# Performance work log

Hardware: AMD Instinct MI355X
Metric: run time of the kernel (lower is better)

## Reference

```python
import jax, jax.numpy as jnp
import numpy as np

N_NODES = 100000
N_EDGES = 1600000
C_IN = 128
C_OUT = 128
BN_EPS = 1e-5


def setup_inputs() -> dict:
    key = jax.random.key(0)
    k = jax.random.split(key, 4)
    x = jax.random.normal(k[0], (N_NODES, C_IN), dtype=jnp.float32)
    edge_index = jax.random.randint(k[1], (2, N_EDGES), 0, N_NODES, dtype=jnp.int32)
    # nn.Linear params (Kaiming-uniform-ish scale)
    lim = 1.0 / np.sqrt(C_IN)
    W = jax.random.uniform(k[2], (C_IN, C_OUT), jnp.float32, -lim, lim)
    b = jnp.zeros((C_OUT,), jnp.float32)
    # BatchNorm (eval mode: running stats)
    gamma = jnp.ones((C_OUT,), jnp.float32)
    beta = jnp.zeros((C_OUT,), jnp.float32)
    running_mean = jnp.zeros((C_OUT,), jnp.float32)
    running_var = jnp.ones((C_OUT,), jnp.float32)
    return {"x": x, "edge_index": edge_index, "W": W, "b": b,
            "gamma": gamma, "beta": beta,
            "running_mean": running_mean, "running_var": running_var}


def reference(x, edge_index, W, b, gamma, beta, running_mean, running_var):
    # Linear projection: [N, C_in] @ [C_in, C_out]
    h = x @ W + b
    in_node, out_node = edge_index[0], edge_index[1]
    # gather edge features then scatter-mean onto destination nodes
    sums = jax.ops.segment_sum(h[in_node], out_node, num_segments=N_NODES)
    cnt = jax.ops.segment_sum(jnp.ones((in_node.shape[0],), h.dtype), out_node,
                              num_segments=N_NODES)
    agg = sums / jnp.maximum(cnt, 1.0)[:, None]  # mean; 0 for isolated nodes
    # BatchNorm1d (eval mode: running stats) + ReLU; dropout is identity in eval
    inv = jax.lax.rsqrt(running_var + BN_EPS)
    out = (agg - running_mean) * (inv * gamma) + beta
    return jax.nn.relu(out)
```

## Files before the change

kernel.cpp:

```cpp
#include <hip/hip_runtime.h>


#define NN 100000
#define NE 1600000
#define CC 128
#define BN_EPS 1e-5f
#define LBLK 1563
#define LSTR 136
#define NBUK 256
#define DPB 391
#define ACH 4096
#define ABLK 391
#define CAP 10240

typedef __attribute__((ext_vector_type(8))) short bf16x8;
typedef __attribute__((ext_vector_type(4))) float f32x4;

static __device__ __forceinline__ short f2bf(float f) {
  union { float f; unsigned u; } v; v.f = f;
  unsigned r = (v.u + 0x7FFF + ((v.u >> 16) & 1)) >> 16;
  return (short)r;
}
static __device__ __forceinline__ float bflo(unsigned p) {
  return __uint_as_float(p << 16);
}
static __device__ __forceinline__ float bfhi(unsigned p) {
  return __uint_as_float(p & 0xffff0000u);
}

static __device__ __forceinline__ int excl_scan256(int* a, int t, int v) {
  a[t] = v;
  __syncthreads();
  for (int d = 1; d < 256; d <<= 1) {
    const int x = (t >= d) ? a[t - d] : 0;
    __syncthreads();
    a[t] += x;
    __syncthreads();
  }
  const int incl = a[t];
  __syncthreads();
  a[t] = incl - v;
  __syncthreads();
  return incl - v;
}

__global__ __launch_bounds__(256) void prep_hist(
    const float* __restrict__ W, const float* __restrict__ bias,
    const float* __restrict__ gamma, const float* __restrict__ beta,
    const float* __restrict__ rmean, const float* __restrict__ rvar,
    const int* __restrict__ ei, short* __restrict__ Wsw,
    float* __restrict__ scsh, int* __restrict__ bhist) {
  __shared__ int lh[NBUK];
  const int t = threadIdx.x;
  const int i = blockIdx.x * 256 + t;
  if (i < CC * CC) {
    const int k = i >> 7, n = i & 127;
    const int nt = n & 7, m = n >> 3;
    const int kb = k >> 5, q = (k >> 3) & 3, j = k & 7;
    Wsw[(size_t)(((nt * 4 + kb) * 64 + (m + 16 * q)) * 8 + j)] = f2bf(W[i]);
  }
  if (i < CC) {
    const float sc = gamma[i] * rsqrtf(rvar[i] + BN_EPS);
    scsh[i] = sc;
    scsh[CC + i] = beta[i] - rmean[i] * sc;
    scsh[2 * CC + i] = bias[i];
  }
  lh[t] = 0;
  __syncthreads();
  const int e0 = blockIdx.x * ACH;
  const int e1 = min(NE, e0 + ACH);
  for (int e = e0 + t; e < e1; e += 256) atomicAdd(&lh[ei[NE + e] / DPB], 1);
  __syncthreads();
  if (lh[t]) atomicAdd(&bhist[t], lh[t]);
}

__global__ __launch_bounds__(256) void scatter_linear(
    const int* __restrict__ ei, const int* __restrict__ bhist,
    int* __restrict__ gcurz, int2* __restrict__ ebuf,
    const float* __restrict__ x, const short* __restrict__ Wsw,
    const float* __restrict__ scsh, short* __restrict__ hout,
    int scat) {
  __shared__ int2 sorted[ACH];
  __shared__ int gsc[NBUK], lh[NBUK], lex[NBUK], rb[NBUK], lc[NBUK];
  const int t = threadIdx.x;

  if (blockIdx.x < scat) {
    const int e0 = blockIdx.x * ACH;
    const int e1 = min(NE, e0 + ACH);
    const int gbase = excl_scan256(gsc, t, bhist[t]);
    lh[t] = 0;
    __syncthreads();
    for (int e = e0 + t; e < e1; e += 256) atomicAdd(&lh[ei[NE + e] / DPB], 1);
    __syncthreads();
    const int vh = lh[t];
    const int lbase = excl_scan256(lex, t, vh);
    lc[t] = lbase;
    if (vh > 0) rb[t] = gbase + atomicAdd(&gcurz[t], vh);
    __syncthreads();
    for (int e = e0 + t; e < e1; e += 256) {
      const int src = ei[e], dst = ei[NE + e];
      const int p = atomicAdd(&lc[dst / DPB], 1);
      sorted[p] = make_int2(src, dst);
    }
    __syncthreads();
    const int n = e1 - e0;
    for (int i = t; i < n; i += 256) {
      const int2 v = sorted[i];
      const int b = v.y / DPB;
      ebuf[rb[b] + (i - lex[b])] = v;
    }
    return;
  }

  short* lsA = (short*)sorted;
  const int n0 = (blockIdx.x - scat) * 64;

#pragma unroll
  for (int j = 0; j < 8; ++j) {
    const int idx = j * 256 + t;
    const int row = idx >> 5, kc4 = idx & 31;
    float4 v = make_float4(0.f, 0.f, 0.f, 0.f);
    if (n0 + row < NN) v = *(const float4*)(x + (size_t)(n0 + row) * CC + kc4 * 4);
    short4 sv;
    sv.x = f2bf(v.x); sv.y = f2bf(v.y); sv.z = f2bf(v.z); sv.w = f2bf(v.w);
    *(short4*)(lsA + row * LSTR + kc4 * 4) = sv;
  }
  __syncthreads();

  const int wave = t >> 6, lane = t & 63;
  const int quad = lane >> 4, m = lane & 15;
  const int rowbase = n0 + wave * 16;

  f32x4 acc[8];
#pragma unroll
  for (int nt = 0; nt < 8; ++nt) acc[nt] = (f32x4){0.f, 0.f, 0.f, 0.f};

#pragma unroll
  for (int kb = 0; kb < 4; ++kb) {
    const bf16x8 a =
        *(const bf16x8*)(lsA + (wave * 16 + m) * LSTR + kb * 32 + quad * 8);
#pragma unroll
    for (int nt = 0; nt < 8; ++nt) {
      bf16x8 bb = *(const bf16x8*)(Wsw + (size_t)(((nt * 4 + kb) * 64 + lane) * 8));
      acc[nt] = __builtin_amdgcn_mfma_f32_16x16x32_bf16(a, bb, acc[nt], 0, 0, 0);
    }
  }

  const float4 b0 = *(const float4*)(scsh + 2 * CC + m * 8);
  const float4 b1 = *(const float4*)(scsh + 2 * CC + m * 8 + 4);
  const float bv[8] = {b0.x, b0.y, b0.z, b0.w, b1.x, b1.y, b1.z, b1.w};

  short* hg = hout + (size_t)(m >> 1) * (NN * 16) + (m & 1) * 8;
#pragma unroll
  for (int reg = 0; reg < 4; ++reg) {
    const int R = rowbase + quad * 4 + reg;
    if (R >= NN) continue;
    bf16x8 hv;
#pragma unroll
    for (int nt = 0; nt < 8; ++nt) hv[nt] = f2bf(acc[nt][reg] + bv[nt]);
    *(bf16x8*)(hg + (size_t)R * 16) = hv;
  }
}

__global__ __launch_bounds__(1024) void bucket_to_csr(
    const int2* __restrict__ ebuf, const int* __restrict__ bhist,
    int* __restrict__ off, int* __restrict__ csr) {
  __shared__ int gs[NBUK];
  __shared__ int dh[512];
  __shared__ int s[512];
  __shared__ int lcur[512];
  __shared__ int lcsr[CAP];
  const int b = blockIdx.x, t = threadIdx.x;

  if (t < NBUK) gs[t] = bhist[t];
  __syncthreads();
  for (int d = 1; d < NBUK; d <<= 1) {
    int a0 = 0;
    if (t < NBUK && t >= d) a0 = gs[t - d];
    __syncthreads();
    if (t < NBUK) gs[t] += a0;
    __syncthreads();
  }
  const int seglen = bhist[b];
  const int segbase = gs[b] - seglen;
  const int lo = b * DPB;
  const int hi = min(NN, lo + DPB);
  const int nd = hi - lo;
  const int2* eb = ebuf + segbase;

  if (t < 512) dh[t] = 0;
  __syncthreads();
  for (int i = t; i < seglen; i += 1024) atomicAdd(&dh[eb[i].y - lo], 1);
  __syncthreads();

  if (t < 512) s[t] = dh[t];
  __syncthreads();
  for (int d = 1; d < 512; d <<= 1) {
    int a0 = 0;
    if (t < 512 && t >= d) a0 = s[t - d];
    __syncthreads();
    if (t < 512) s[t] += a0;
    __syncthreads();
  }
  if (t < 512) lcur[t] = s[t] - dh[t];
  if (t < nd) off[lo + t] = segbase + (s[t] - dh[t]);
  if (b == NBUK - 1 && t == 0) off[NN] = NE;
  __syncthreads();

  if (seglen <= CAP) {
    for (int i = t; i < seglen; i += 1024) {
      const int2 e = eb[i];
      const int p = atomicAdd(&lcur[e.y - lo], 1);
      lcsr[p] = e.x;
    }
    __syncthreads();
    for (int i = t; i < seglen; i += 1024) csr[segbase + i] = lcsr[i];
  } else {
    for (int i = t; i < seglen; i += 1024) {
      const int2 e = eb[i];
      const int p = atomicAdd(&lcur[e.y - lo], 1);
      csr[segbase + p] = e.x;
    }
  }
}

__global__ __launch_bounds__(256) void gather_bn_relu(
    const short* __restrict__ h, const int* __restrict__ off,
    const int* __restrict__ csr, const float* __restrict__ scsh,
    float* __restrict__ out) {
  const int g = blockIdx.x & 7;
  const int wave = threadIdx.x >> 6, lane = threadIdx.x & 63;
  const int o = lane >> 3, c8 = lane & 7;
  const int node = (blockIdx.x >> 3) * 32 + wave * 8 + o;
  const unsigned* hb = (const unsigned*)h + (size_t)g * (NN * 8) + c8;

  int s = 0, e = 0;
  if (node < NN) { s = off[node]; e = off[node + 1]; }

  float ax = 0.f, ay = 0.f;
  int i = s;
  for (; i + 4 <= e; i += 4) {
    const int s0 = csr[i + 0], s1 = csr[i + 1];
    const int s2 = csr[i + 2], s3 = csr[i + 3];
    const unsigned p0 = hb[(size_t)s0 * 8];
    const unsigned p1 = hb[(size_t)s1 * 8];
    const unsigned p2 = hb[(size_t)s2 * 8];
    const unsigned p3 = hb[(size_t)s3 * 8];
    ax += (bflo(p0) + bflo(p1)) + (bflo(p2) + bflo(p3));
    ay += (bfhi(p0) + bfhi(p1)) + (bfhi(p2) + bfhi(p3));
  }
  for (; i < e; ++i) {
    const unsigned p = hb[(size_t)csr[i] * 8];
    ax += bflo(p);
    ay += bfhi(p);
  }
  if (node < NN) {
    const float inv = (e > s) ? 1.0f / (float)(e - s) : 0.0f;
    const int cidx = g * 16 + c8 * 2;
    const float2 sc = *(const float2*)(scsh + cidx);
    const float2 sh = *(const float2*)(scsh + CC + cidx);
    float2 o2;
    o2.x = fmaxf(0.f, ax * inv * sc.x + sh.x);
    o2.y = fmaxf(0.f, ay * inv * sc.y + sh.y);
    *(float2*)(out + (size_t)node * CC + cidx) = o2;
  }
}

__global__ __launch_bounds__(256) void edge_scatter(
    const float* __restrict__ x, const int* __restrict__ ei,
    float* __restrict__ sums, int* __restrict__ cnt) {
  int gt = blockIdx.x * 256 + threadIdx.x;
  int e = gt >> 5;
  int sub = gt & 31;
  if (e >= NE) return;
  int src = ei[e];
  int dst = ei[NE + e];
  const float4 v = *(const float4*)(x + (size_t)src * CC + sub * 4);
  float* o = sums + (size_t)dst * CC + sub * 4;
  unsafeAtomicAdd(o + 0, v.x);
  unsafeAtomicAdd(o + 1, v.y);
  unsafeAtomicAdd(o + 2, v.z);
  unsafeAtomicAdd(o + 3, v.w);
  if (sub == 0) atomicAdd(cnt + dst, 1);
}

__global__ __launch_bounds__(256) void gemm_bn_relu_fb(
    float* buf, const float* __restrict__ W, const float* __restrict__ bias,
    const float* __restrict__ gamma, const float* __restrict__ beta,
    const float* __restrict__ rmean, const float* __restrict__ rvar,
    const int* __restrict__ cnt) {
  __shared__ float xsT[CC][65];
  const int t = threadIdx.x;
  const int n0 = blockIdx.x * 64;
  for (int j = 0; j < 8; ++j) {
    int i = t + 256 * j;
    int row = i >> 5;
    int ko = (i & 31) * 4;
    float4 v = make_float4(0.f, 0.f, 0.f, 0.f);
    if (n0 + row < NN) v = *(const float4*)(buf + (size_t)(n0 + row) * CC + ko);
    xsT[ko + 0][row] = v.x;
    xsT[ko + 1][row] = v.y;
    xsT[ko + 2][row] = v.z;
    xsT[ko + 3][row] = v.w;
  }
  __syncthreads();
  const int cg = t & 31;
  const int ng8 = (t >> 5) * 8;
  float acc[8][4];
#pragma unroll
  for (int j = 0; j < 8; ++j)
#pragma unroll
    for (int c = 0; c < 4; ++c) acc[j][c] = 0.f;
#pragma unroll 8
  for (int k = 0; k < CC; ++k) {
    const float4 wv = *(const float4*)(W + k * CC + cg * 4);
#pragma unroll
    for (int j = 0; j < 8; ++j) {
      const float xv = xsT[k][ng8 + j];
      acc[j][0] = fmaf(xv, wv.x, acc[j][0]);
      acc[j][1] = fmaf(xv, wv.y, acc[j][1]);
      acc[j][2] = fmaf(xv, wv.z, acc[j][2]);
      acc[j][3] = fmaf(xv, wv.w, acc[j][3]);
    }
  }
  const float4 bb = *(const float4*)(bias + cg * 4);
  const float4 gg = *(const float4*)(gamma + cg * 4);
  const float4 bt = *(const float4*)(beta + cg * 4);
  const float4 mu = *(const float4*)(rmean + cg * 4);
  const float4 vr = *(const float4*)(rvar + cg * 4);
  float sc[4], sh[4];
  sc[0] = gg.x * rsqrtf(vr.x + BN_EPS);
  sc[1] = gg.y * rsqrtf(vr.y + BN_EPS);
  sc[2] = gg.z * rsqrtf(vr.z + BN_EPS);
  sc[3] = gg.w * rsqrtf(vr.w + BN_EPS);
  sh[0] = bt.x - mu.x * sc[0];
  sh[1] = bt.y - mu.y * sc[1];
  sh[2] = bt.z - mu.z * sc[2];
  sh[3] = bt.w - mu.w * sc[3];
#pragma unroll
  for (int j = 0; j < 8; ++j) {
    const int n = n0 + ng8 + j;
    if (n >= NN) continue;
    const int cn = cnt[n];
    const float inv = cn > 0 ? 1.0f / (float)cn : 0.0f;
    const float bsel = cn > 0 ? 1.0f : 0.0f;
    float4 o;
    o.x = fmaxf(0.f, (acc[j][0] * inv + bsel * bb.x) * sc[0] + sh[0]);
    o.y = fmaxf(0.f, (acc[j][1] * inv + bsel * bb.y) * sc[1] + sh[1]);
    o.z = fmaxf(0.f, (acc[j][2] * inv + bsel * bb.z) * sc[2] + sh[2]);
    o.w = fmaxf(0.f, (acc[j][3] * inv + bsel * bb.w) * sc[3] + sh[3]);
    *(float4*)(buf + (size_t)n * CC + cg * 4) = o;
  }
}

extern "C" void kernel_launch(void* const* d_in, const int* in_sizes, int n_in,
                              void* d_out, int out_size, void* d_ws, size_t ws_size,
                              hipStream_t stream) {
  const float* x     = (const float*)d_in[0];
  const int*   ei    = (const int*)d_in[1];
  const float* W     = (const float*)d_in[2];
  const float* bias  = (const float*)d_in[3];
  const float* gamma = (const float*)d_in[4];
  const float* beta  = (const float*)d_in[5];
  const float* rmean = (const float*)d_in[6];
  const float* rvar  = (const float*)d_in[7];
  float* out = (float*)d_out;

  const size_t OFF_B  = 0;
  const size_t BH_B   = 400128;
  const size_t GC_B   = 401152;
  const size_t CSR_B  = 802304;
  const size_t SCSH_B = 7202304;
  const size_t WSW_B  = 7204352;
  const size_t EB_B   = 7237120;
  const size_t H1_B   = 20037120;
  const size_t NEED1  = H1_B + (size_t)NN * CC * 2;
  const size_t NEED2  = EB_B + (size_t)NN * CC * 2;

  const int GGRID = ((NN + 31) / 32) * 8;

  if (ws_size >= NEED2) {
    int*   off   = (int*)((char*)d_ws + OFF_B);
    int*   bhist = (int*)((char*)d_ws + BH_B);
    int*   gcurz = (int*)((char*)d_ws + GC_B);
    int*   csr   = (int*)((char*)d_ws + CSR_B);
    float* scsh  = (float*)((char*)d_ws + SCSH_B);
    short* Wsw   = (short*)((char*)d_ws + WSW_B);

    hipMemsetAsync(bhist, 0, 2048, stream);
    prep_hist<<<ABLK, 256, 0, stream>>>(W, bias, gamma, beta, rmean, rvar,
                                        ei, Wsw, scsh, bhist);
    if (ws_size >= NEED1) {
      int2*  ebuf = (int2*)((char*)d_ws + EB_B);
      short* h    = (short*)((char*)d_ws + H1_B);
      scatter_linear<<<ABLK + LBLK, 256, 0, stream>>>(
          ei, bhist, gcurz, ebuf, x, Wsw, scsh, h, ABLK);
      bucket_to_csr<<<NBUK, 1024, 0, stream>>>(ebuf, bhist, off, csr);
      gather_bn_relu<<<GGRID, 256, 0, stream>>>(h, off, csr, scsh, out);
    } else {
      int2*  ebuf = (int2*)((char*)d_ws + EB_B);
      short* h    = (short*)((char*)d_ws + EB_B);
      scatter_linear<<<ABLK, 256, 0, stream>>>(
          ei, bhist, gcurz, ebuf, x, Wsw, scsh, h, ABLK);
      bucket_to_csr<<<NBUK, 1024, 0, stream>>>(ebuf, bhist, off, csr);
      scatter_linear<<<LBLK, 256, 0, stream>>>(
          ei, bhist, gcurz, ebuf, x, Wsw, scsh, h, 0);
      gather_bn_relu<<<GGRID, 256, 0, stream>>>(h, off, csr, scsh, out);
    }
  } else {
    int* cnt = (int*)d_ws;
    hipMemsetAsync(out, 0, (size_t)NN * CC * sizeof(float), stream);
    hipMemsetAsync(cnt, 0, (size_t)NN * sizeof(int), stream);
    edge_scatter<<<(NE * 32) / 256, 256, 0, stream>>>(x, ei, out, cnt);
    gemm_bn_relu_fb<<<(NN + 63) / 64, 256, 0, stream>>>(
        out, W, bias, gamma, beta, rmean, rvar, cnt);
  }
}
```

Measured before the change: 255.3 us.

## Stage CSR segments in LDS and widen per-thread gather in aggregation kernel

Measured after the change: 238.7 us. -6.5%, faster.

```diff
diff --git a/kernel.cpp b/kernel.cpp
--- a/kernel.cpp
+++ b/kernel.cpp
@@ -12,6 +12,8 @@
 #define ACH 4096
 #define ABLK 391
 #define CAP 10240
+#define GNB 256
+#define CAP2 5120
 
 typedef __attribute__((ext_vector_type(8))) short bf16x8;
 typedef __attribute__((ext_vector_type(4))) float f32x4;
@@ -129,7 +131,6 @@
 
   const int wave = t >> 6, lane = t & 63;
   const int quad = lane >> 4, m = lane & 15;
-  const int rowbase = n0 + wave * 16;
 
   f32x4 acc[8];
 #pragma unroll
@@ -150,15 +151,28 @@
   const float4 b1 = *(const float4*)(scsh + 2 * CC + m * 8 + 4);
   const float bv[8] = {b0.x, b0.y, b0.z, b0.w, b1.x, b1.y, b1.z, b1.w};
 
-  short* hg = hout + (size_t)(m >> 1) * (NN * 16) + (m & 1) * 8;
+  __syncthreads();
+
 #pragma unroll
   for (int reg = 0; reg < 4; ++reg) {
-    const int R = rowbase + quad * 4 + reg;
-    if (R >= NN) continue;
+    const int r = wave * 16 + quad * 4 + reg;
     bf16x8 hv;
 #pragma unroll
     for (int nt = 0; nt < 8; ++nt) hv[nt] = f2bf(acc[nt][reg] + bv[nt]);
-    *(bf16x8*)(hg + (size_t)R * 16) = hv;
+    *(bf16x8*)(lsA + r * LSTR + m * 8) = hv;
+  }
+  __syncthreads();
+
+#pragma unroll
+  for (int rr = 0; rr < 4; ++rr) {
+    const int g2 = rr * 2 + (t >> 7);
+    const int idx = t & 127;
+    const int row = idx >> 1, half = idx & 1;
+    const int R = n0 + row;
+    if (R < NN) {
+      bf16x8 v = *(const bf16x8*)(lsA + row * LSTR + g2 * 16 + half * 8);
+      *(bf16x8*)(hout + (size_t)g2 * (NN * 16) + (size_t)R * 16 + half * 8) = v;
+    }
   }
 }
 
@@ -228,41 +242,83 @@
     const short* __restrict__ h, const int* __restrict__ off,
     const int* __restrict__ csr, const float* __restrict__ scsh,
     float* __restrict__ out) {
+  __shared__ int loff[GNB + 1];
+  __shared__ int lcsr[CAP2];
   const int g = blockIdx.x & 7;
-  const int wave = threadIdx.x >> 6, lane = threadIdx.x & 63;
-  const int o = lane >> 3, c8 = lane & 7;
-  const int node = (blockIdx.x >> 3) * 32 + wave * 8 + o;
-  const unsigned* hb = (const unsigned*)h + (size_t)g * (NN * 8) + c8;
-
-  int s = 0, e = 0;
-  if (node < NN) { s = off[node]; e = off[node + 1]; }
-
-  float ax = 0.f, ay = 0.f;
-  int i = s;
-  for (; i + 4 <= e; i += 4) {
-    const int s0 = csr[i + 0], s1 = csr[i + 1];
-    const int s2 = csr[i + 2], s3 = csr[i + 3];
-    const unsigned p0 = hb[(size_t)s0 * 8];
-    const unsigned p1 = hb[(size_t)s1 * 8];
-    const unsigned p2 = hb[(size_t)s2 * 8];
-    const unsigned p3 = hb[(size_t)s3 * 8];
-    ax += (bflo(p0) + bflo(p1)) + (bflo(p2) + bflo(p3));
-    ay += (bfhi(p0) + bfhi(p1)) + (bfhi(p2) + bfhi(p3));
-  }
-  for (; i < e; ++i) {
-    const unsigned p = hb[(size_t)csr[i] * 8];
-    ax += bflo(p);
-    ay += bfhi(p);
-  }
-  if (node < NN) {
-    const float inv = (e > s) ? 1.0f / (float)(e - s) : 0.0f;
-    const int cidx = g * 16 + c8 * 2;
-    const float2 sc = *(const float2*)(scsh + cidx);
-    const float2 sh = *(const float2*)(scsh + CC + cidx);
-    float2 o2;
-    o2.x = fmaxf(0.f, ax * inv * sc.x + sh.x);
-    o2.y = fmaxf(0.f, ay * inv * sc.y + sh.y);
-    *(float2*)(out + (size_t)node * CC + cidx) = o2;
+  const int nb0 = (blockIdx.x >> 3) * GNB;
+  const int t = threadIdx.x;
+  const int nnb = min(GNB, NN - nb0);
+
+  for (int i = t; i <= nnb; i += 256) loff[i] = off[nb0 + i];
+  __syncthreads();
+  const int s0 = loff[0];
+  const int seglen = loff[nnb] - s0;
+  const int stg = min(seglen, CAP2);
+  for (int i = t; i < stg; i += 256) lcsr[i] = csr[s0 + i];
+  __syncthreads();
+
+  const int c4 = t & 3;
+  const int lgid = t >> 2;
+  const short* hg = h + (size_t)g * (NN * 16);
+  const float4 sc = *(const float4*)(scsh + g * 16 + c4 * 4);
+  const float4 sh = *(const float4*)(scsh + CC + g * 16 + c4 * 4);
+
+  if (seglen <= CAP2) {
+#pragma unroll
+    for (int nn = 0; nn < 4; ++nn) {
+      const int l = lgid * 4 + nn;
+      if (l < nnb) {
+        const int s = loff[l] - s0, e = loff[l + 1] - s0;
+        float a0 = 0.f, a1 = 0.f, a2 = 0.f, a3 = 0.f;
+        int i = s;
+        for (; i + 4 <= e; i += 4) {
+          const int e0 = lcsr[i], e1 = lcsr[i + 1];
+          const int e2 = lcsr[i + 2], e3 = lcsr[i + 3];
+          const uint2 p0 = *(const uint2*)(hg + (size_t)e0 * 16 + c4 * 4);
+          const uint2 p1 = *(const uint2*)(hg + (size_t)e1 * 16 + c4 * 4);
+          const uint2 p2 = *(const uint2*)(hg + (size_t)e2 * 16 + c4 * 4);
+          const uint2 p3 = *(const uint2*)(hg + (size_t)e3 * 16 + c4 * 4);
+          a0 += (bflo(p0.x) + bflo(p1.x)) + (bflo(p2.x) + bflo(p3.x));
+          a1 += (bfhi(p0.x) + bfhi(p1.x)) + (bfhi(p2.x) + bfhi(p3.x));
+          a2 += (bflo(p0.y) + bflo(p1.y)) + (bflo(p2.y) + bflo(p3.y));
+          a3 += (bfhi(p0.y) + bfhi(p1.y)) + (bfhi(p2.y) + bfhi(p3.y));
+        }
+        for (; i < e; ++i) {
+          const uint2 p = *(const uint2*)(hg + (size_t)lcsr[i] * 16 + c4 * 4);
+          a0 += bflo(p.x); a1 += bfhi(p.x);
+          a2 += bflo(p.y); a3 += bfhi(p.y);
+        }
+        const int node = nb0 + l;
+        const float inv = (e > s) ? 1.0f / (float)(e - s) : 0.0f;
+        float4 o;
+        o.x = fmaxf(0.f, a0 * inv * sc.x + sh.x);
+        o.y = fmaxf(0.f, a1 * inv * sc.y + sh.y);
+        o.z = fmaxf(0.f, a2 * inv * sc.z + sh.z);
+        o.w = fmaxf(0.f, a3 * inv * sc.w + sh.w);
+        *(float4*)(out + (size_t)node * CC + g * 16 + c4 * 4) = o;
+      }
+    }
+  } else {
+    for (int nn = 0; nn < 4; ++nn) {
+      const int l = lgid * 4 + nn;
+      if (l < nnb) {
+        const int s = loff[l], e = loff[l + 1];
+        float a0 = 0.f, a1 = 0.f, a2 = 0.f, a3 = 0.f;
+        for (int i = s; i < e; ++i) {
+          const uint2 p = *(const uint2*)(hg + (size_t)csr[i] * 16 + c4 * 4);
+          a0 += bflo(p.x); a1 += bfhi(p.x);
+          a2 += bflo(p.y); a3 += bfhi(p.y);
+        }
+        const int node = nb0 + l;
+        const float inv = (e > s) ? 1.0f / (float)(e - s) : 0.0f;
+        float4 o;
+        o.x = fmaxf(0.f, a0 * inv * sc.x + sh.x);
+        o.y = fmaxf(0.f, a1 * inv * sc.y + sh.y);
+        o.z = fmaxf(0.f, a2 * inv * sc.z + sh.z);
+        o.w = fmaxf(0.f, a3 * inv * sc.w + sh.w);
+        *(float4*)(out + (size_t)node * CC + g * 16 + c4 * 4) = o;
+      }
+    }
   }
 }
 
@@ -377,7 +433,7 @@
   const size_t NEED1  = H1_B + (size_t)NN * CC * 2;
   const size_t NEED2  = EB_B + (size_t)NN * CC * 2;
 
-  const int GGRID = ((NN + 31) / 32) * 8;
+  const int GGRID = ((NN + GNB - 1) / GNB) * 8;
 
   if (ws_size >= NEED2) {
     int*   off   = (int*)((char*)d_ws + OFF_B);
```

## Store h row-major and gather full 256-byte rows per edge with staged CSR

Applied to the files above, without the earlier changes.

Measured after the change: 222.3 us. 1.15x faster.

```diff
diff --git a/kernel.cpp b/kernel.cpp
--- a/kernel.cpp
+++ b/kernel.cpp
@@ -12,6 +12,8 @@
 #define ACH 4096
 #define ABLK 391
 #define CAP 10240
+#define GNB 64
+#define CAP2 1536
 
 typedef __attribute__((ext_vector_type(8))) short bf16x8;
 typedef __attribute__((ext_vector_type(4))) float f32x4;
@@ -150,7 +152,6 @@
   const float4 b1 = *(const float4*)(scsh + 2 * CC + m * 8 + 4);
   const float bv[8] = {b0.x, b0.y, b0.z, b0.w, b1.x, b1.y, b1.z, b1.w};
 
-  short* hg = hout + (size_t)(m >> 1) * (NN * 16) + (m & 1) * 8;
 #pragma unroll
   for (int reg = 0; reg < 4; ++reg) {
     const int R = rowbase + quad * 4 + reg;
@@ -158,7 +159,7 @@
     bf16x8 hv;
 #pragma unroll
     for (int nt = 0; nt < 8; ++nt) hv[nt] = f2bf(acc[nt][reg] + bv[nt]);
-    *(bf16x8*)(hg + (size_t)R * 16) = hv;
+    *(bf16x8*)(hout + (size_t)R * CC + m * 8) = hv;
   }
 }
 
@@ -228,41 +229,77 @@
     const short* __restrict__ h, const int* __restrict__ off,
     const int* __restrict__ csr, const float* __restrict__ scsh,
     float* __restrict__ out) {
-  const int g = blockIdx.x & 7;
-  const int wave = threadIdx.x >> 6, lane = threadIdx.x & 63;
-  const int o = lane >> 3, c8 = lane & 7;
-  const int node = (blockIdx.x >> 3) * 32 + wave * 8 + o;
-  const unsigned* hb = (const unsigned*)h + (size_t)g * (NN * 8) + c8;
-
-  int s = 0, e = 0;
-  if (node < NN) { s = off[node]; e = off[node + 1]; }
-
-  float ax = 0.f, ay = 0.f;
-  int i = s;
-  for (; i + 4 <= e; i += 4) {
-    const int s0 = csr[i + 0], s1 = csr[i + 1];
-    const int s2 = csr[i + 2], s3 = csr[i + 3];
-    const unsigned p0 = hb[(size_t)s0 * 8];
-    const unsigned p1 = hb[(size_t)s1 * 8];
-    const unsigned p2 = hb[(size_t)s2 * 8];
-    const unsigned p3 = hb[(size_t)s3 * 8];
-    ax += (bflo(p0) + bflo(p1)) + (bflo(p2) + bflo(p3));
-    ay += (bfhi(p0) + bfhi(p1)) + (bfhi(p2) + bfhi(p3));
-  }
-  for (; i < e; ++i) {
-    const unsigned p = hb[(size_t)csr[i] * 8];
-    ax += bflo(p);
-    ay += bfhi(p);
-  }
-  if (node < NN) {
-    const float inv = (e > s) ? 1.0f / (float)(e - s) : 0.0f;
-    const int cidx = g * 16 + c8 * 2;
-    const float2 sc = *(const float2*)(scsh + cidx);
-    const float2 sh = *(const float2*)(scsh + CC + cidx);
-    float2 o2;
-    o2.x = fmaxf(0.f, ax * inv * sc.x + sh.x);
-    o2.y = fmaxf(0.f, ay * inv * sc.y + sh.y);
-    *(float2*)(out + (size_t)node * CC + cidx) = o2;
+  __shared__ int loff[GNB + 1];
+  __shared__ int lcsr[CAP2];
+  const int nb0 = blockIdx.x * GNB;
+  const int t = threadIdx.x;
+  const int nnb = min(GNB, NN - nb0);
+
+  for (int i = t; i <= nnb; i += 256) loff[i] = off[nb0 + i];
+  __syncthreads();
+  const int s0 = loff[0];
+  const int seglen = loff[nnb] - s0;
+  const int stg = min(seglen, CAP2);
+  for (int i = t; i < stg; i += 256) lcsr[i] = csr[s0 + i];
+  __syncthreads();
+
+  const int wave = t >> 6, lane = t & 63;
+  const int e4 = lane >> 4;
+  const int c16 = lane & 15;
+  const float4 sc0 = *(const float4*)(scsh + c16 * 8);
+  const float4 sc1 = *(const float4*)(scsh + c16 * 8 + 4);
+  const float4 sh0 = *(const float4*)(scsh + CC + c16 * 8);
+  const float4 sh1 = *(const float4*)(scsh + CC + c16 * 8 + 4);
+
+  const int lEnd = min(nnb, wave * 16 + 16);
+  const bool inl = (seglen <= CAP2);
+  for (int l = wave * 16; l < lEnd; ++l) {
+    const int s = inl ? loff[l] - s0 : loff[l];
+    const int e = inl ? loff[l + 1] - s0 : loff[l + 1];
+    float a0 = 0.f, a1 = 0.f, a2 = 0.f, a3 = 0.f;
+    float a4 = 0.f, a5 = 0.f, a6 = 0.f, a7 = 0.f;
+    int i = s + e4;
+    for (; i + 4 < e; i += 8) {
+      const int q0 = inl ? lcsr[i] : csr[i];
+      const int q1 = inl ? lcsr[i + 4] : csr[i + 4];
+      const uint4 p0 = *(const uint4*)(h + (size_t)q0 * CC + c16 * 8);
+      const uint4 p1 = *(const uint4*)(h + (size_t)q1 * CC + c16 * 8);
+      a0 += bflo(p0.x) + bflo(p1.x); a1 += bfhi(p0.x) + bfhi(p1.x);
+      a2 += bflo(p0.y) + bflo(p1.y); a3 += bfhi(p0.y) + bfhi(p1.y);
+      a4 += bflo(p0.z) + bflo(p1.z); a5 += bfhi(p0.z) + bfhi(p1.z);
+      a6 += bflo(p0.w) + bflo(p1.w); a7 += bfhi(p0.w) + bfhi(p1.w);
+    }
+    if (i < e) {
+      const int q = inl ? lcsr[i] : csr[i];
+      const uint4 p = *(const uint4*)(h + (size_t)q * CC + c16 * 8);
+      a0 += bflo(p.x); a1 += bfhi(p.x);
+      a2 += bflo(p.y); a3 += bfhi(p.y);
+      a4 += bflo(p.z); a5 += bfhi(p.z);
+      a6 += bflo(p.w); a7 += bfhi(p.w);
+    }
+    a0 += __shfl_xor(a0, 16); a1 += __shfl_xor(a1, 16);
+    a2 += __shfl_xor(a2, 16); a3 += __shfl_xor(a3, 16);
+    a4 += __shfl_xor(a4, 16); a5 += __shfl_xor(a5, 16);
+    a6 += __shfl_xor(a6, 16); a7 += __shfl_xor(a7, 16);
+    a0 += __shfl_xor(a0, 32); a1 += __shfl_xor(a1, 32);
+    a2 += __shfl_xor(a2, 32); a3 += __shfl_xor(a3, 32);
+    a4 += __shfl_xor(a4, 32); a5 += __shfl_xor(a5, 32);
+    a6 += __shfl_xor(a6, 32); a7 += __shfl_xor(a7, 32);
+    if (e4 == 0) {
+      const float inv = (e > s) ? 1.0f / (float)(e - s) : 0.0f;
+      float4 o0, o1;
+      o0.x = fmaxf(0.f, a0 * inv * sc0.x + sh0.x);
+      o0.y = fmaxf(0.f, a1 * inv * sc0.y + sh0.y);
+      o0.z = fmaxf(0.f, a2 * inv * sc0.z + sh0.z);
+      o0.w = fmaxf(0.f, a3 * inv * sc0.w + sh0.w);
+      o1.x = fmaxf(0.f, a4 * inv * sc1.x + sh1.x);
+      o1.y = fmaxf(0.f, a5 * inv * sc1.y + sh1.y);
+      o1.z = fmaxf(0.f, a6 * inv * sc1.z + sh1.z);
+      o1.w = fmaxf(0.f, a7 * inv * sc1.w + sh1.w);
+      float* op = out + (size_t)(nb0 + l) * CC + c16 * 8;
+      *(float4*)op = o0;
+      *(float4*)(op + 4) = o1;
+    }
   }
 }
 
@@ -377,7 +414,7 @@
   const size_t NEED1  = H1_B + (size_t)NN * CC * 2;
   const size_t NEED2  = EB_B + (size_t)NN * CC * 2;
 
-  const int GGRID = ((NN + 31) / 32) * 8;
+  const int GGRID = (NN + GNB - 1) / GNB;
 
   if (ws_size >= NEED2) {
     int*   off   = (int*)((char*)d_ws + OFF_B);
```
